# Performance work log

Measured on AMD Instinct MI355X. Metric: run time of the kernel, lower is better.

## Reference

```python
import jax, jax.numpy as jnp
import numpy as np

EPS = 1e-12

def l2norm(v, axis):
    return v / jnp.maximum(jnp.linalg.norm(v, axis=axis, keepdims=True), EPS)

def setup_inputs() -> dict:
    key = jax.random.key(0)
    k1, k2, k3, k4 = jax.random.split(key, 4)
    N, C, S, K = 16, 128, 16384, 64
    return {
        "x": jax.random.normal(k1, (N, C, S), dtype=jnp.float32),
        "fc_w": jax.random.normal(k2, (K, C), dtype=jnp.float32),
        "fc_b": jax.random.normal(k3, (K,), dtype=jnp.float32),
        "centroids": jax.random.uniform(k4, (K, C), dtype=jnp.float32),
    }

def reference(x, fc_w, fc_b, centroids):
    # x: [N, C, S]; fc_w: [K, C]; centroids: [K, C]
    x = l2norm(x, axis=1)  # descriptor-wise L2 normalize over channels
    # 1x1 conv (per-position linear) -> soft assignment over clusters
    logits = jnp.einsum('ncs,kc->nks', x, fc_w) + fc_b[None, :, None]
    soft = jax.nn.softmax(logits, axis=1)  # [N, K, S]
    # vlad[n,k,c] = sum_s soft[n,k,s] * (x[n,c,s] - centroids[k,c])
    # matmul decomposition avoids materializing [N,K,C,S]
    a_sum = soft.sum(axis=-1)  # [N, K]
    vlad = jnp.einsum('nks,ncs->nkc', soft, x) - a_sum[:, :, None] * centroids[None]
    vlad = l2norm(vlad, axis=2)            # intra-normalization
    vlad = vlad.reshape(vlad.shape[0], -1)  # [N, K*C]
    vlad = l2norm(vlad, axis=1)            # final L2 normalize
    return vlad
```

## Files before the change

### kernel.cpp

```cpp
#include <hip/hip_runtime.h>
#include <hip/hip_fp16.h>

#define N_ 16
#define C_ 128
#define S_ 16384
#define K_ 64

typedef __attribute__((ext_vector_type(4))) float f32x4;
typedef __attribute__((ext_vector_type(8))) _Float16 f16x8;
typedef __attribute__((ext_vector_type(4))) _Float16 f16x4;

#define SWZ_S(s) ((((s) ^ ((s) >> 3)) & 7) << 3)

__global__ __launch_bounds__(256, 2) void fused_kernel(
    const float* __restrict__ x, const float* __restrict__ fc_w,
    const float* __restrict__ fc_b, float* __restrict__ vlad_acc,
    float* __restrict__ a_sum)
{
    __shared__ _Float16 xT[64 * 128];
    __shared__ _Float16 xC[128 * 64];
    __shared__ _Float16 Wh[64 * 128];
    __shared__ _Float16 Wl[64 * 128];
    __shared__ _Float16 sst[64 * 64];
    __shared__ float rns[8][64];

    const int tid = threadIdx.x;
    const int n = blockIdx.x >> 5;
    const int chunk = blockIdx.x & 31;
    const int lane = tid & 63, w = tid >> 6;
    const int lr = lane & 15, g = lane >> 4;
    const int fsw = (lr & 7) << 3;

#pragma unroll
    for (int i = 0; i < 8; ++i) {
        int idx = i * 256 + tid;
        int c4 = idx & 31, k = idx >> 5;
        float4 wv = *(const float4*)(fc_w + k * C_ + c4 * 4);
        _Float16 h0 = (_Float16)wv.x, h1 = (_Float16)wv.y,
                 h2 = (_Float16)wv.z, h3 = (_Float16)wv.w;
        f16x4 hi = {h0, h1, h2, h3};
        f16x4 lo = {(_Float16)(wv.x - (float)h0), (_Float16)(wv.y - (float)h1),
                    (_Float16)(wv.z - (float)h2), (_Float16)(wv.w - (float)h3)};
        int e = k * 128 + ((c4 * 4) ^ ((k & 7) << 3));
        *(f16x4*)&Wh[e] = hi;
        *(f16x4*)&Wl[e] = lo;
    }
    {
        float* rp = &rns[0][0];
        rp[tid] = 0.f;
        rp[256 + tid] = 0.f;
    }

    float bias[4];
#pragma unroll
    for (int nt = 0; nt < 4; ++nt) bias[nt] = fc_b[nt * 16 + lr];
    float a_acc[4] = {0.f, 0.f, 0.f, 0.f};
    f32x4 vacc[8];
#pragma unroll
    for (int nt = 0; nt < 8; ++nt) vacc[nt] = (f32x4){0.f, 0.f, 0.f, 0.f};

    const float* xb = x + (size_t)n * C_ * S_;
    const int s4 = tid & 15;
    int cqv[2];
#pragma unroll
    for (int i = 0; i < 2; ++i) cqv[i] = i * 16 + (tid >> 4);

    float4 pre[2][4];
#pragma unroll
    for (int i = 0; i < 2; ++i)
#pragma unroll
        for (int cc = 0; cc < 4; ++cc)
            pre[i][cc] = *(const float4*)(xb + (size_t)(cqv[i] * 4 + cc) * S_ +
                                          chunk * 512 + s4 * 4);

#pragma unroll 1
    for (int t = 0; t < 8; ++t) {
        __syncthreads();
        float part[4] = {0.f, 0.f, 0.f, 0.f};
#pragma unroll
        for (int i = 0; i < 2; ++i) {
            int cq = cqv[i];
#pragma unroll
            for (int j = 0; j < 4; ++j) {
                float v0 = (&pre[i][0].x)[j], v1 = (&pre[i][1].x)[j],
                      v2 = (&pre[i][2].x)[j], v3 = (&pre[i][3].x)[j];
                part[j] += v0 * v0 + v1 * v1 + v2 * v2 + v3 * v3;
                f16x4 p = {(_Float16)v0, (_Float16)v1, (_Float16)v2, (_Float16)v3};
                int s = s4 * 4 + j;
                *(f16x4*)&xT[s * 128 + ((cq * 4) ^ SWZ_S(s))] = p;
            }
#pragma unroll
            for (int cc = 0; cc < 4; ++cc) {
                int c = cq * 4 + cc;
                f16x4 q = {(_Float16)pre[i][cc].x, (_Float16)pre[i][cc].y,
                           (_Float16)pre[i][cc].z, (_Float16)pre[i][cc].w};
                *(f16x4*)&xC[c * 64 + ((s4 * 4) ^ ((c & 7) << 3))] = q;
            }
        }
#pragma unroll
        for (int j = 0; j < 4; ++j) {
            part[j] += __shfl_xor(part[j], 16);
            part[j] += __shfl_xor(part[j], 32);
        }
        if (g == 0) {
#pragma unroll
            for (int j = 0; j < 4; ++j)
                atomicAdd(&rns[t][lr * 4 + j], part[j]);
        }
        if (t < 7) {
#pragma unroll
            for (int i = 0; i < 2; ++i)
#pragma unroll
                for (int cc = 0; cc < 4; ++cc)
                    pre[i][cc] = *(const float4*)(xb + (size_t)(cqv[i] * 4 + cc) * S_ +
                                                  chunk * 512 + (t + 1) * 64 + s4 * 4);
        }
        __syncthreads();

        f32x4 acc[4];
#pragma unroll
        for (int nt = 0; nt < 4; ++nt) acc[nt] = (f32x4){0.f, 0.f, 0.f, 0.f};
#pragma unroll
        for (int kt = 0; kt < 4; ++kt) {
            const int co = kt * 32 + g * 8;
            const int sa = w * 16 + lr;
            f16x8 af = *(const f16x8*)&xT[sa * 128 + (co ^ SWZ_S(sa))];
            f16x8 whf[4], wlf[4];
#pragma unroll
            for (int nt = 0; nt < 4; ++nt) {
                int e = (nt * 16 + lr) * 128 + (co ^ fsw);
                whf[nt] = *(const f16x8*)&Wh[e];
                wlf[nt] = *(const f16x8*)&Wl[e];
            }
#pragma unroll
            for (int nt = 0; nt < 4; ++nt) {
                acc[nt] = __builtin_amdgcn_mfma_f32_16x16x32_f16(af, whf[nt], acc[nt], 0, 0, 0);
                acc[nt] = __builtin_amdgcn_mfma_f32_16x16x32_f16(af, wlf[nt], acc[nt], 0, 0, 0);
            }
        }

        {
            float rnl[4], ai[4];
#pragma unroll
            for (int r = 0; r < 4; ++r) {
                float ss = rns[t][w * 16 + g * 4 + r];
                rnl[r] = 1.0f / fmaxf(sqrtf(ss), 1e-12f);
            }
#pragma unroll
            for (int nt = 0; nt < 4; ++nt)
#pragma unroll
                for (int r = 0; r < 4; ++r)
                    acc[nt][r] = __expf(acc[nt][r] * rnl[r] + bias[nt]);
#pragma unroll
            for (int r = 0; r < 4; ++r) {
                float sum = (acc[0][r] + acc[1][r]) + (acc[2][r] + acc[3][r]);
                sum += __shfl_xor(sum, 1);
                sum += __shfl_xor(sum, 2);
                sum += __shfl_xor(sum, 4);
                sum += __shfl_xor(sum, 8);
                float bi = 1.0f / sum;
                ai[r] = bi * rnl[r];
#pragma unroll
                for (int nt = 0; nt < 4; ++nt) a_acc[nt] += acc[nt][r] * bi;
            }
#pragma unroll
            for (int nt = 0; nt < 4; ++nt) {
                int k = nt * 16 + lr;
                int sloc = w * 16 + g * 4;
                f16x4 p = {(_Float16)(acc[nt][0] * ai[0]), (_Float16)(acc[nt][1] * ai[1]),
                           (_Float16)(acc[nt][2] * ai[2]), (_Float16)(acc[nt][3] * ai[3])};
                *(f16x4*)&sst[k * 64 + (sloc ^ ((k & 7) << 3))] = p;
            }
        }
        __syncthreads();

#pragma unroll
        for (int kt = 0; kt < 2; ++kt) {
            const int so = kt * 32 + g * 8;
            f16x8 pa = *(const f16x8*)&sst[(w * 16 + lr) * 64 + (so ^ fsw)];
#pragma unroll
            for (int nt = 0; nt < 8; ++nt) {
                f16x8 xv = *(const f16x8*)&xC[(nt * 16 + lr) * 64 + (so ^ fsw)];
                vacc[nt] = __builtin_amdgcn_mfma_f32_16x16x32_f16(pa, xv, vacc[nt], 0, 0, 0);
            }
        }
    }

    float* vp = vlad_acc + ((size_t)n * K_ + w * 16) * C_;
#pragma unroll
    for (int nt = 0; nt < 8; ++nt)
#pragma unroll
        for (int r = 0; r < 4; ++r)
            atomicAdd(vp + (g * 4 + r) * C_ + nt * 16 + lr, vacc[nt][r]);
#pragma unroll
    for (int nt = 0; nt < 4; ++nt) {
        a_acc[nt] += __shfl_xor(a_acc[nt], 16);
        a_acc[nt] += __shfl_xor(a_acc[nt], 32);
    }
    if (lane < 16) {
#pragma unroll
        for (int nt = 0; nt < 4; ++nt)
            atomicAdd(a_sum + n * K_ + nt * 16 + lr, a_acc[nt]);
    }
}

__global__ __launch_bounds__(256) void finalize_kernel(
    const float* __restrict__ vlad_acc, const float* __restrict__ a_sum,
    const float* __restrict__ centroids, float* __restrict__ out)
{
    __shared__ float red[4];
    const int n = blockIdx.x;
    const int t = threadIdx.x;
    const int k = t >> 2, q = t & 3;
    const float av = a_sum[n * K_ + k];
    const float* vp = vlad_acc + ((size_t)n * K_ + k) * C_;
    const float* cp = centroids + k * C_;

    float v[32];
    float ssq = 0.f;
#pragma unroll
    for (int j = 0; j < 32; ++j) {
        int c = q + 4 * j;
        float val = vp[c] - av * cp[c];
        v[j] = val;
        ssq += val * val;
    }
    ssq += __shfl_xor(ssq, 1);
    ssq += __shfl_xor(ssq, 2);
    const float inv1 = 1.0f / fmaxf(sqrtf(ssq), 1e-12f);

    float gp = (q == 0) ? ssq * inv1 * inv1 : 0.f;
#pragma unroll
    for (int off = 1; off < 64; off <<= 1) gp += __shfl_xor(gp, off);
    if ((t & 63) == 0) red[t >> 6] = gp;
    __syncthreads();
    const float G = red[0] + red[1] + red[2] + red[3];
    const float ginv = 1.0f / fmaxf(sqrtf(G), 1e-12f);

    float* op = out + (size_t)n * (K_ * C_) + k * C_;
#pragma unroll
    for (int j = 0; j < 32; ++j) op[q + 4 * j] = v[j] * inv1 * ginv;
}

extern "C" void kernel_launch(void* const* d_in, const int* in_sizes, int n_in,
                              void* d_out, int out_size, void* d_ws, size_t ws_size,
                              hipStream_t stream) {
    const float* x     = (const float*)d_in[0];
    const float* fc_w  = (const float*)d_in[1];
    const float* fc_b  = (const float*)d_in[2];
    const float* cent  = (const float*)d_in[3];
    float* out = (float*)d_out;

    char* ws = (char*)d_ws;
    float* a_sum = (float*)ws;
    float* vlad  = (float*)(ws + 4096);

    hipMemsetAsync(ws, 0, 4096 + (size_t)N_ * K_ * C_ * sizeof(float), stream);

    fused_kernel<<<N_ * 32, 256, 0, stream>>>(x, fc_w, fc_b, vlad, a_sum);
    finalize_kernel<<<N_, 256, 0, stream>>>(vlad, a_sum, cent, out);
}
```

Measured before the change: 60.39 us.

## Drop split-fp16 weights, double-buffer xC, replace atomics with partial-sum reduction

The fc weights now live in registers as single fp16 fragments, which drops the hi/lo split and halves the logits MFMAs. The xC tile is double-buffered so each step's VLAD MFMA runs one iteration late and overlaps the next tile's load, removing one barrier per iteration. Global atomics and the memset give way to per-block partial writes plus a separate reduce kernel, and the finalize kernel is widened to 1024 threads. The cost is lower logit precision from dropping the fp16 low-part correction, an extra kernel launch, and roughly 16 MB of partial traffic through workspace.

New measurement: 51.95 us. 14.0% less time.

```diff
diff --git a/kernel.cpp b/kernel.cpp
--- a/kernel.cpp
+++ b/kernel.cpp
@@ -14,13 +14,11 @@
 
 __global__ __launch_bounds__(256, 2) void fused_kernel(
     const float* __restrict__ x, const float* __restrict__ fc_w,
-    const float* __restrict__ fc_b, float* __restrict__ vlad_acc,
-    float* __restrict__ a_sum)
+    const float* __restrict__ fc_b, float* __restrict__ vlad_part,
+    float* __restrict__ a_part)
 {
     __shared__ _Float16 xT[64 * 128];
-    __shared__ _Float16 xC[128 * 64];
-    __shared__ _Float16 Wh[64 * 128];
-    __shared__ _Float16 Wl[64 * 128];
+    __shared__ _Float16 xC[2][128 * 64];
     __shared__ _Float16 sst[64 * 64];
     __shared__ float rns[8][64];
 
@@ -31,20 +29,22 @@
     const int lr = lane & 15, g = lane >> 4;
     const int fsw = (lr & 7) << 3;
 
-#pragma unroll
-    for (int i = 0; i < 8; ++i) {
-        int idx = i * 256 + tid;
-        int c4 = idx & 31, k = idx >> 5;
-        float4 wv = *(const float4*)(fc_w + k * C_ + c4 * 4);
-        _Float16 h0 = (_Float16)wv.x, h1 = (_Float16)wv.y,
-                 h2 = (_Float16)wv.z, h3 = (_Float16)wv.w;
-        f16x4 hi = {h0, h1, h2, h3};
-        f16x4 lo = {(_Float16)(wv.x - (float)h0), (_Float16)(wv.y - (float)h1),
-                    (_Float16)(wv.z - (float)h2), (_Float16)(wv.w - (float)h3)};
-        int e = k * 128 + ((c4 * 4) ^ ((k & 7) << 3));
-        *(f16x4*)&Wh[e] = hi;
-        *(f16x4*)&Wl[e] = lo;
-    }
+    f16x8 wfrag[4][4];
+#pragma unroll
+    for (int nt = 0; nt < 4; ++nt)
+#pragma unroll
+        for (int kt = 0; kt < 4; ++kt) {
+            const float* wp = fc_w + (nt * 16 + lr) * C_ + kt * 32 + g * 8;
+            float4 wa = *(const float4*)wp;
+            float4 wb = *(const float4*)(wp + 4);
+            f16x8 f;
+            f[0] = (_Float16)wa.x; f[1] = (_Float16)wa.y;
+            f[2] = (_Float16)wa.z; f[3] = (_Float16)wa.w;
+            f[4] = (_Float16)wb.x; f[5] = (_Float16)wb.y;
+            f[6] = (_Float16)wb.z; f[7] = (_Float16)wb.w;
+            wfrag[nt][kt] = f;
+        }
+
     {
         float* rp = &rns[0][0];
         rp[tid] = 0.f;
@@ -75,7 +75,9 @@
 
 #pragma unroll 1
     for (int t = 0; t < 8; ++t) {
+        const int b = t & 1;
         __syncthreads();
+
         float part[4] = {0.f, 0.f, 0.f, 0.f};
 #pragma unroll
         for (int i = 0; i < 2; ++i) {
@@ -94,7 +96,7 @@
                 int c = cq * 4 + cc;
                 f16x4 q = {(_Float16)pre[i][cc].x, (_Float16)pre[i][cc].y,
                            (_Float16)pre[i][cc].z, (_Float16)pre[i][cc].w};
-                *(f16x4*)&xC[c * 64 + ((s4 * 4) ^ ((c & 7) << 3))] = q;
+                *(f16x4*)&xC[b][c * 64 + ((s4 * 4) ^ ((c & 7) << 3))] = q;
             }
         }
 #pragma unroll
@@ -114,6 +116,20 @@
                 for (int cc = 0; cc < 4; ++cc)
                     pre[i][cc] = *(const float4*)(xb + (size_t)(cqv[i] * 4 + cc) * S_ +
                                                   chunk * 512 + (t + 1) * 64 + s4 * 4);
+        }
+
+        if (t > 0) {
+            const _Float16* xcp = xC[b ^ 1];
+#pragma unroll
+            for (int kt = 0; kt < 2; ++kt) {
+                const int so = kt * 32 + g * 8;
+                f16x8 pa = *(const f16x8*)&sst[(w * 16 + lr) * 64 + (so ^ fsw)];
+#pragma unroll
+                for (int nt = 0; nt < 8; ++nt) {
+                    f16x8 xv = *(const f16x8*)&xcp[(nt * 16 + lr) * 64 + (so ^ fsw)];
+                    vacc[nt] = __builtin_amdgcn_mfma_f32_16x16x32_f16(pa, xv, vacc[nt], 0, 0, 0);
+                }
+            }
         }
         __syncthreads();
 
@@ -125,18 +141,9 @@
             const int co = kt * 32 + g * 8;
             const int sa = w * 16 + lr;
             f16x8 af = *(const f16x8*)&xT[sa * 128 + (co ^ SWZ_S(sa))];
-            f16x8 whf[4], wlf[4];
-#pragma unroll
-            for (int nt = 0; nt < 4; ++nt) {
-                int e = (nt * 16 + lr) * 128 + (co ^ fsw);
-                whf[nt] = *(const f16x8*)&Wh[e];
-                wlf[nt] = *(const f16x8*)&Wl[e];
-            }
-#pragma unroll
-            for (int nt = 0; nt < 4; ++nt) {
-                acc[nt] = __builtin_amdgcn_mfma_f32_16x16x32_f16(af, whf[nt], acc[nt], 0, 0, 0);
-                acc[nt] = __builtin_amdgcn_mfma_f32_16x16x32_f16(af, wlf[nt], acc[nt], 0, 0, 0);
-            }
+#pragma unroll
+            for (int nt = 0; nt < 4; ++nt)
+                acc[nt] = __builtin_amdgcn_mfma_f32_16x16x32_f16(af, wfrag[nt][kt], acc[nt], 0, 0, 0);
         }
 
         {
@@ -172,26 +179,28 @@
                 *(f16x4*)&sst[k * 64 + (sloc ^ ((k & 7) << 3))] = p;
             }
         }
-        __syncthreads();
-
+    }
+
+    __syncthreads();
+    {
+        const _Float16* xcp = xC[1];
 #pragma unroll
         for (int kt = 0; kt < 2; ++kt) {
             const int so = kt * 32 + g * 8;
             f16x8 pa = *(const f16x8*)&sst[(w * 16 + lr) * 64 + (so ^ fsw)];
 #pragma unroll
             for (int nt = 0; nt < 8; ++nt) {
-                f16x8 xv = *(const f16x8*)&xC[(nt * 16 + lr) * 64 + (so ^ fsw)];
+                f16x8 xv = *(const f16x8*)&xcp[(nt * 16 + lr) * 64 + (so ^ fsw)];
                 vacc[nt] = __builtin_amdgcn_mfma_f32_16x16x32_f16(pa, xv, vacc[nt], 0, 0, 0);
             }
         }
     }
-
-    float* vp = vlad_acc + ((size_t)n * K_ + w * 16) * C_;
+    float* vp = vlad_part + (size_t)blockIdx.x * (K_ * C_) + (w * 16) * C_;
 #pragma unroll
     for (int nt = 0; nt < 8; ++nt)
 #pragma unroll
         for (int r = 0; r < 4; ++r)
-            atomicAdd(vp + (g * 4 + r) * C_ + nt * 16 + lr, vacc[nt][r]);
+            vp[(g * 4 + r) * C_ + nt * 16 + lr] = vacc[nt][r];
 #pragma unroll
     for (int nt = 0; nt < 4; ++nt) {
         a_acc[nt] += __shfl_xor(a_acc[nt], 16);
@@ -200,33 +209,59 @@
     if (lane < 16) {
 #pragma unroll
         for (int nt = 0; nt < 4; ++nt)
-            atomicAdd(a_sum + n * K_ + nt * 16 + lr, a_acc[nt]);
-    }
-}
-
-__global__ __launch_bounds__(256) void finalize_kernel(
-    const float* __restrict__ vlad_acc, const float* __restrict__ a_sum,
+            a_part[blockIdx.x * 256 + w * 64 + nt * 16 + lr] = a_acc[nt];
+    }
+}
+
+__global__ __launch_bounds__(256) void reduce_kernel(
+    const float* __restrict__ vlad_part, float* __restrict__ vlad_sum)
+{
+    const int n = blockIdx.x >> 5, g8 = blockIdx.x & 31;
+    const int e = g8 * 256 + threadIdx.x;
+    const float* p = vlad_part + (size_t)(n * 32) * (K_ * C_) + e;
+    float acc = 0.f;
+#pragma unroll
+    for (int ch = 0; ch < 32; ++ch) acc += p[(size_t)ch * (K_ * C_)];
+    vlad_sum[n * (K_ * C_) + e] = acc;
+}
+
+__global__ __launch_bounds__(1024) void finalize_kernel(
+    const float* __restrict__ vlad_sum, const float* __restrict__ a_part,
     const float* __restrict__ centroids, float* __restrict__ out)
 {
-    __shared__ float red[4];
+    __shared__ float red[16];
     const int n = blockIdx.x;
     const int t = threadIdx.x;
-    const int k = t >> 2, q = t & 3;
-    const float av = a_sum[n * K_ + k];
-    const float* vp = vlad_acc + ((size_t)n * K_ + k) * C_;
+    const int k = t >> 4, q = t & 15;
+
+    float av = 0.f;
+#pragma unroll
+    for (int cc = 0; cc < 2; ++cc) {
+        int ch = q * 2 + cc;
+        const float* ap = a_part + (size_t)(n * 32 + ch) * 256 + k;
+#pragma unroll
+        for (int ww = 0; ww < 4; ++ww) av += ap[ww * 64];
+    }
+    av += __shfl_xor(av, 1);
+    av += __shfl_xor(av, 2);
+    av += __shfl_xor(av, 4);
+    av += __shfl_xor(av, 8);
+
+    const float* vp = vlad_sum + (size_t)n * (K_ * C_) + k * C_;
     const float* cp = centroids + k * C_;
-
-    float v[32];
+    float v[8];
     float ssq = 0.f;
 #pragma unroll
-    for (int j = 0; j < 32; ++j) {
-        int c = q + 4 * j;
+    for (int j = 0; j < 8; ++j) {
+        int c = q + 16 * j;
         float val = vp[c] - av * cp[c];
         v[j] = val;
         ssq += val * val;
     }
     ssq += __shfl_xor(ssq, 1);
     ssq += __shfl_xor(ssq, 2);
+    ssq += __shfl_xor(ssq, 4);
+    ssq += __shfl_xor(ssq, 8);
     const float inv1 = 1.0f / fmaxf(sqrtf(ssq), 1e-12f);
 
     float gp = (q == 0) ? ssq * inv1 * inv1 : 0.f;
@@ -234,12 +269,14 @@
     for (int off = 1; off < 64; off <<= 1) gp += __shfl_xor(gp, off);
     if ((t & 63) == 0) red[t >> 6] = gp;
     __syncthreads();
-    const float G = red[0] + red[1] + red[2] + red[3];
+    float G = 0.f;
+#pragma unroll
+    for (int i = 0; i < 16; ++i) G += red[i];
     const float ginv = 1.0f / fmaxf(sqrtf(G), 1e-12f);
 
     float* op = out + (size_t)n * (K_ * C_) + k * C_;
 #pragma unroll
-    for (int j = 0; j < 32; ++j) op[q + 4 * j] = v[j] * inv1 * ginv;
+    for (int j = 0; j < 8; ++j) op[q + 16 * j] = v[j] * inv1 * ginv;
 }
 
 extern "C" void kernel_launch(void* const* d_in, const int* in_sizes, int n_in,
@@ -252,11 +289,11 @@
     float* out = (float*)d_out;
 
     char* ws = (char*)d_ws;
-    float* a_sum = (float*)ws;
-    float* vlad  = (float*)(ws + 4096);
-
-    hipMemsetAsync(ws, 0, 4096 + (size_t)N_ * K_ * C_ * sizeof(float), stream);
-
-    fused_kernel<<<N_ * 32, 256, 0, stream>>>(x, fc_w, fc_b, vlad, a_sum);
-    finalize_kernel<<<N_, 256, 0, stream>>>(vlad, a_sum, cent, out);
-}
+    float* vlad_part = (float*)ws;
+    float* a_part    = (float*)(ws + (size_t)512 * K_ * C_ * 4);
+    float* vlad_sum  = (float*)(ws + (size_t)512 * K_ * C_ * 4 + 512 * 1024);
+
+    fused_kernel<<<N_ * 32, 256, 0, stream>>>(x, fc_w, fc_b, vlad_part, a_part);
+    reduce_kernel<<<N_ * 32, 256, 0, stream>>>(vlad_part, vlad_sum);
+    finalize_kernel<<<N_, 1024, 0, stream>>>(vlad_sum, a_part, cent, out);
+}
```
